# Kernel tuning notes

Hardware: AMD Instinct MI355X
Metric: run time of the kernel (lower is better)

The kernel has to match this reference:

```python
import jax, jax.numpy as jnp
import numpy as np

N_NODES = 100000
N_EDGES = 1600000
IN_DIM = 128
OUT_DIM = 128
LEAKY_SLOPE = 0.01  # torch nn.LeakyReLU default


def setup_inputs() -> dict:
    key = jax.random.key(0)
    k1, k2, k3, k4 = jax.random.split(key, 4)
    x = jax.random.normal(k1, (N_NODES, IN_DIM), dtype=jnp.float32)
    edge_index = jax.random.randint(k2, (2, N_EDGES), 0, N_NODES, dtype=jnp.int64)
    edge_attr = jax.random.uniform(k3, (N_EDGES,), dtype=jnp.float32)
    # Linear params (xavier_uniform weight, zero bias)
    limit = np.sqrt(6.0 / (IN_DIM + OUT_DIM)).astype(np.float32)
    W = jax.random.uniform(k4, (OUT_DIM, IN_DIM), minval=-limit, maxval=limit, dtype=jnp.float32)
    b = jnp.zeros((OUT_DIM,), dtype=jnp.float32)
    return {"x": x, "edge_index": edge_index, "edge_attr": edge_attr, "W": W, "b": b}


def reference(x, edge_index, edge_attr, W, b):
    src = edge_index[0]  # x_j (source nodes)
    dst = edge_index[1]  # aggregation index (target nodes)
    # message: gather source features, scale by per-edge scalar  [E, D]
    msg = x[src] * edge_attr[:, None]
    # aggregate: scatter-add over target index  [N, D]
    agg = jax.ops.segment_sum(msg, dst, num_segments=N_NODES)
    # update: Linear + LeakyReLU (dropout is identity at p=0 / eval)
    out = agg @ W.T + b
    return jnp.where(out >= 0, out, LEAKY_SLOPE * out)
```

## Files before the change

### kernel.cpp

```cpp
#include <hip/hip_runtime.h>

#define N_NODES 100000
#define N_EDGES 1600000
#define DIM 128
#define LEAKY 0.01f
#define RS_STRIDE 132
#define WS_STRIDE 132
#define NBUCKET 391
#define SB_EDGES 4096
#define NSB 391

typedef short bf16x8 __attribute__((ext_vector_type(8)));
typedef float f32x4 __attribute__((ext_vector_type(4)));

static __device__ __forceinline__ unsigned short f2bf(float f) {
  unsigned int u = __float_as_uint(f);
  u = (u + 0x7fffu + ((u >> 16) & 1u)) >> 16;
  return (unsigned short)u;
}

__global__ __launch_bounds__(512) void sort_local_kernel(
    const int* __restrict__ ei, const float* __restrict__ attr,
    int2* __restrict__ binned, unsigned short* __restrict__ counts,
    int* __restrict__ srcOff) {
  __shared__ int hist[NBUCKET];
  __shared__ int cursor[NBUCKET];
  __shared__ int scanBuf[512];
  __shared__ int2 stage[SB_EDGES];

  const int t = threadIdx.x;
  const int blk = blockIdx.x;
  const int base = blk * SB_EDGES;
  const int n = min(SB_EDGES, N_EDGES - base);

  if (t < NBUCKET) hist[t] = 0;
  __syncthreads();

  int myP[8];
  int myB[8];
  float myA[8];
#pragma unroll
  for (int k = 0; k < 8; ++k) {
    int i = t + k * 512;
    if (i < n) {
      int e = base + i;
      int s = ei[e];
      int d = ei[N_EDGES + e];
      myA[k] = attr[e];
      myB[k] = d >> 8;
      myP[k] = s | ((d & 255) << 17);
      atomicAdd(&hist[myB[k]], 1);
    } else {
      myB[k] = -1;
    }
  }
  __syncthreads();

  int v = (t < NBUCKET) ? hist[t] : 0;
  scanBuf[t] = v;
  __syncthreads();
  for (int off = 1; off < 512; off <<= 1) {
    int u = (t >= off) ? scanBuf[t - off] : 0;
    __syncthreads();
    scanBuf[t] += u;
    __syncthreads();
  }
  if (t < NBUCKET) {
    int excl = scanBuf[t] - v;
    cursor[t] = excl;
    counts[(size_t)t * NSB + blk] = (unsigned short)v;
    srcOff[(size_t)t * NSB + blk] = base + excl;
  }
  __syncthreads();

#pragma unroll
  for (int k = 0; k < 8; ++k) {
    if (myB[k] >= 0) {
      int loc = atomicAdd(&cursor[myB[k]], 1);
      stage[loc] = make_int2(myP[k], __float_as_int(myA[k]));
    }
  }
  __syncthreads();

  for (int i = t; i < n; i += 512) binned[base + i] = stage[i];
}

__global__ __launch_bounds__(128) void bucket_count_kernel(
    const unsigned short* __restrict__ counts, int* __restrict__ bucketCount) {
  __shared__ int red[128];
  const int b = blockIdx.x;
  const int t = threadIdx.x;
  int s = 0;
  for (int sb = t; sb < NSB; sb += 128) s += counts[(size_t)b * NSB + sb];
  red[t] = s;
  __syncthreads();
  for (int off = 64; off > 0; off >>= 1) {
    if (t < off) red[t] += red[t + off];
    __syncthreads();
  }
  if (t == 0) bucketCount[b] = red[0];
}

__global__ __launch_bounds__(512) void bucket_scan_kernel(
    const int* __restrict__ bucketCount, int* __restrict__ bucketBase) {
  __shared__ int s[512];
  const int t = threadIdx.x;
  int v = (t < NBUCKET) ? bucketCount[t] : 0;
  s[t] = v;
  __syncthreads();
  for (int off = 1; off < 512; off <<= 1) {
    int u = (t >= off) ? s[t - off] : 0;
    __syncthreads();
    s[t] += u;
    __syncthreads();
  }
  if (t < NBUCKET) bucketBase[t] = s[t] - v;
}

__global__ __launch_bounds__(512) void passB_kernel(
    const int2* __restrict__ binned, const unsigned short* __restrict__ counts,
    const int* __restrict__ srcOff, const int* __restrict__ bucketBase,
    int2* __restrict__ csr, int* __restrict__ row_ptr) {
  __shared__ int runPrefix[NSB + 1];
  __shared__ int runSrc[NSB];
  __shared__ int hist[256];
  __shared__ int nodeBase[256];
  __shared__ int cur[256];
  __shared__ int scanBuf[512];

  const int b = blockIdx.x;
  const int t = threadIdx.x;

  if (t < NSB) runSrc[t] = srcOff[(size_t)b * NSB + t];
  int len = (t < NSB) ? (int)counts[(size_t)b * NSB + t] : 0;
  scanBuf[t] = len;
  __syncthreads();
  for (int off = 1; off < 512; off <<= 1) {
    int u = (t >= off) ? scanBuf[t - off] : 0;
    __syncthreads();
    scanBuf[t] += u;
    __syncthreads();
  }
  if (t < NSB) runPrefix[t] = scanBuf[t] - len;
  if (t == NSB) runPrefix[NSB] = scanBuf[NSB];
  if (t < 256) hist[t] = 0;
  __syncthreads();

  const int total = runPrefix[NSB];

  for (int i = t; i < total; i += 512) {
    int lo = 0, hi = NSB - 1;
    while (lo < hi) {
      int mid = (lo + hi + 1) >> 1;
      if (runPrefix[mid] <= i) lo = mid; else hi = mid - 1;
    }
    int px = binned[runSrc[lo] + (i - runPrefix[lo])].x;
    atomicAdd(&hist[(px >> 17) & 255], 1);
  }
  __syncthreads();

  int hv = (t < 256) ? hist[t] : 0;
  scanBuf[t] = hv;
  __syncthreads();
  for (int off = 1; off < 512; off <<= 1) {
    int u = (t >= off) ? scanBuf[t - off] : 0;
    __syncthreads();
    scanBuf[t] += u;
    __syncthreads();
  }
  const int bb = bucketBase[b];
  if (t < 256) {
    int excl = scanBuf[t] - hv;
    nodeBase[t] = excl;
    cur[t] = excl;
    int node = b * 256 + t;
    if (node < N_NODES) row_ptr[node] = bb + excl;
  }
  if (b == 0 && t == 0) row_ptr[N_NODES] = N_EDGES;
  __syncthreads();

  for (int i = t; i < total; i += 512) {
    int lo = 0, hi = NSB - 1;
    while (lo < hi) {
      int mid = (lo + hi + 1) >> 1;
      if (runPrefix[mid] <= i) lo = mid; else hi = mid - 1;
    }
    int2 rec = binned[runSrc[lo] + (i - runPrefix[lo])];
    int ld = (rec.x >> 17) & 255;
    int pos = bb + atomicAdd(&cur[ld], 1);
    csr[pos] = make_int2(rec.x & 0x1FFFF, rec.y);
  }
}

__global__ __launch_bounds__(256) void x2b_kernel(
    const float4* __restrict__ x, ushort4* __restrict__ xb) {
  const int i = blockIdx.x * 256 + threadIdx.x;
  float4 v = x[i];
  ushort4 o;
  o.x = f2bf(v.x); o.y = f2bf(v.y); o.z = f2bf(v.z); o.w = f2bf(v.w);
  xb[i] = o;
}

__global__ __launch_bounds__(256) void gather_bf16_kernel(
    const unsigned short* __restrict__ xb, const int* __restrict__ row_ptr,
    const int2* __restrict__ csr, float* __restrict__ out) {
  const int node = blockIdx.x * 4 + (threadIdx.x >> 6);
  const int lane = threadIdx.x & 63;

  const int beg = row_ptr[node];
  const int end = row_ptr[node + 1];

  float2 acc = make_float2(0.f, 0.f);
  int e = beg;
  for (; e + 3 < end; e += 4) {
    int2 e0 = csr[e];
    int2 e1 = csr[e + 1];
    int2 e2 = csr[e + 2];
    int2 e3 = csr[e + 3];
    unsigned int u0 = *(const unsigned int*)(xb + (size_t)e0.x * DIM + lane * 2);
    unsigned int u1 = *(const unsigned int*)(xb + (size_t)e1.x * DIM + lane * 2);
    unsigned int u2 = *(const unsigned int*)(xb + (size_t)e2.x * DIM + lane * 2);
    unsigned int u3 = *(const unsigned int*)(xb + (size_t)e3.x * DIM + lane * 2);
    float a0 = __int_as_float(e0.y), a1 = __int_as_float(e1.y);
    float a2 = __int_as_float(e2.y), a3 = __int_as_float(e3.y);
    acc.x += __uint_as_float(u0 << 16) * a0;
    acc.y += __uint_as_float(u0 & 0xffff0000u) * a0;
    acc.x += __uint_as_float(u1 << 16) * a1;
    acc.y += __uint_as_float(u1 & 0xffff0000u) * a1;
    acc.x += __uint_as_float(u2 << 16) * a2;
    acc.y += __uint_as_float(u2 & 0xffff0000u) * a2;
    acc.x += __uint_as_float(u3 << 16) * a3;
    acc.y += __uint_as_float(u3 & 0xffff0000u) * a3;
  }
  for (; e < end; ++e) {
    int2 e0 = csr[e];
    float a0 = __int_as_float(e0.y);
    unsigned int u0 = *(const unsigned int*)(xb + (size_t)e0.x * DIM + lane * 2);
    acc.x += __uint_as_float(u0 << 16) * a0;
    acc.y += __uint_as_float(u0 & 0xffff0000u) * a0;
  }
  *(float2*)(out + (size_t)node * DIM + lane * 2) = acc;
}

__global__ __launch_bounds__(256) void gather_f32_kernel(
    const float* __restrict__ x, const int* __restrict__ row_ptr,
    const int2* __restrict__ csr, float* __restrict__ out) {
  const int node = blockIdx.x * 4 + (threadIdx.x >> 6);
  const int lane = threadIdx.x & 63;

  const int beg = row_ptr[node];
  const int end = row_ptr[node + 1];

  float2 acc = make_float2(0.f, 0.f);
  int e = beg;
  for (; e + 3 < end; e += 4) {
    int2 e0 = csr[e];
    int2 e1 = csr[e + 1];
    int2 e2 = csr[e + 2];
    int2 e3 = csr[e + 3];
    float2 v0 = *(const float2*)(x + (size_t)e0.x * DIM + lane * 2);
    float2 v1 = *(const float2*)(x + (size_t)e1.x * DIM + lane * 2);
    float2 v2 = *(const float2*)(x + (size_t)e2.x * DIM + lane * 2);
    float2 v3 = *(const float2*)(x + (size_t)e3.x * DIM + lane * 2);
    float a0 = __int_as_float(e0.y), a1 = __int_as_float(e1.y);
    float a2 = __int_as_float(e2.y), a3 = __int_as_float(e3.y);
    acc.x += v0.x * a0; acc.y += v0.y * a0;
    acc.x += v1.x * a1; acc.y += v1.y * a1;
    acc.x += v2.x * a2; acc.y += v2.y * a2;
    acc.x += v3.x * a3; acc.y += v3.y * a3;
  }
  for (; e < end; ++e) {
    int2 e0 = csr[e];
    float a0 = __int_as_float(e0.y);
    float2 v0 = *(const float2*)(x + (size_t)e0.x * DIM + lane * 2);
    acc.x += v0.x * a0; acc.y += v0.y * a0;
  }
  *(float2*)(out + (size_t)node * DIM + lane * 2) = acc;
}

__global__ __launch_bounds__(256) void w_frag_kernel(
    const float* __restrict__ W, bf16x8* __restrict__ wfrag) {
  const int gid = blockIdx.x * 256 + threadIdx.x;
  const int lane = gid & 63;
  const int q = (gid >> 6) & 3;
  const int nt = gid >> 8;
  const int n = nt * 16 + (lane & 15);
  const int kb = q * 32 + ((lane >> 4) & 3) * 8;
  const float4 f0 = *(const float4*)(W + n * DIM + kb);
  const float4 f1 = *(const float4*)(W + n * DIM + kb + 4);
  bf16x8 frag;
  frag[0] = (short)f2bf(f0.x); frag[1] = (short)f2bf(f0.y);
  frag[2] = (short)f2bf(f0.z); frag[3] = (short)f2bf(f0.w);
  frag[4] = (short)f2bf(f1.x); frag[5] = (short)f2bf(f1.y);
  frag[6] = (short)f2bf(f1.z); frag[7] = (short)f2bf(f1.w);
  wfrag[gid] = frag;
}

__global__ __launch_bounds__(256) void linear_mfma_kernel(
    const float* __restrict__ agg, const bf16x8* __restrict__ wfrag,
    const float* __restrict__ bias, float* __restrict__ out) {
  const int wave = threadIdx.x >> 6;
  const int lane = threadIdx.x & 63;
  const int r0 = (blockIdx.x * 4 + wave) * 16;
  if (r0 >= N_NODES) return;

  const int m = lane & 15;
  const int quad = lane >> 4;
  const int row = r0 + m;

  bf16x8 afrag[4];
#pragma unroll
  for (int q = 0; q < 4; ++q) {
    const float* ap = agg + (size_t)row * DIM + q * 32 + quad * 8;
    const float4 f0 = *(const float4*)(ap);
    const float4 f1 = *(const float4*)(ap + 4);
    afrag[q][0] = (short)f2bf(f0.x); afrag[q][1] = (short)f2bf(f0.y);
    afrag[q][2] = (short)f2bf(f0.z); afrag[q][3] = (short)f2bf(f0.w);
    afrag[q][4] = (short)f2bf(f1.x); afrag[q][5] = (short)f2bf(f1.y);
    afrag[q][6] = (short)f2bf(f1.z); afrag[q][7] = (short)f2bf(f1.w);
  }

#pragma unroll
  for (int nt = 0; nt < 8; ++nt) {
    const float bv = bias[nt * 16 + m];
    f32x4 acc = {bv, bv, bv, bv};
#pragma unroll
    for (int q = 0; q < 4; ++q) {
      bf16x8 bfrag = wfrag[(nt * 4 + q) * 64 + lane];
      acc = __builtin_amdgcn_mfma_f32_16x16x32_bf16(afrag[q], bfrag, acc, 0, 0, 0);
    }
    const int col = nt * 16 + m;
#pragma unroll
    for (int i = 0; i < 4; ++i) {
      float v = acc[i];
      v = v >= 0.f ? v : v * LEAKY;
      out[(size_t)(r0 + quad * 4 + i) * DIM + col] = v;
    }
  }
}

__global__ __launch_bounds__(256) void scatter_kernel(
    const float* __restrict__ x, const int* __restrict__ ei,
    const float* __restrict__ attr, float* __restrict__ agg) {
  int gid = blockIdx.x * blockDim.x + threadIdx.x;
  int e = gid >> 5;
  int f = (gid & 31) * 4;
  if (e >= N_EDGES) return;
  int s = ei[e];
  int d = ei[N_EDGES + e];
  float a = attr[e];
  const float4 xv = *(const float4*)(x + (size_t)s * DIM + f);
  float* dp = agg + (size_t)d * DIM + f;
  atomicAdd(dp + 0, xv.x * a);
  atomicAdd(dp + 1, xv.y * a);
  atomicAdd(dp + 2, xv.z * a);
  atomicAdd(dp + 3, xv.w * a);
}

__global__ __launch_bounds__(256, 2) void linear_kernel(
    const float* __restrict__ agg, const float* __restrict__ W,
    const float* __restrict__ bias, float* __restrict__ out) {
  __shared__ float Rs[32 * RS_STRIDE];
  __shared__ float Ws[64 * WS_STRIDE];

  const int tid = threadIdx.x;
  const int c = (tid & 31) * 4;
  const int rg = tid >> 5;
  const size_t rowBase = (size_t)blockIdx.x * 32;

  {
    const int lr = tid >> 3;
    const int col = (tid & 7) * 16;
    const float4* src = (const float4*)(agg + (rowBase + lr) * DIM + col);
#pragma unroll
    for (int j = 0; j < 4; ++j) {
      *(float4*)(Rs + lr * RS_STRIDE + col + j * 4) = src[j];
    }
  }

  const float4 bv = *(const float4*)(bias + c);
  float4 acc0 = bv, acc1 = bv, acc2 = bv, acc3 = bv;

  for (int half = 0; half < 2; ++half) {
    __syncthreads();
    {
      const int k0 = tid >> 7;
      const int o = tid & 127;
#pragma unroll
      for (int kk = k0; kk < 64; kk += 2) {
        Ws[kk * WS_STRIDE + o] = W[o * DIM + half * 64 + kk];
      }
    }
    __syncthreads();

    const float* rs0 = Rs + (rg * 4 + 0) * RS_STRIDE + half * 64;
    const float* rs1 = Rs + (rg * 4 + 1) * RS_STRIDE + half * 64;
    const float* rs2 = Rs + (rg * 4 + 2) * RS_STRIDE + half * 64;
    const float* rs3 = Rs + (rg * 4 + 3) * RS_STRIDE + half * 64;

#pragma unroll 8
    for (int k4 = 0; k4 < 16; ++k4) {
      const float4 v0 = *(const float4*)(rs0 + k4 * 4);
      const float4 v1 = *(const float4*)(rs1 + k4 * 4);
      const float4 v2 = *(const float4*)(rs2 + k4 * 4);
      const float4 v3 = *(const float4*)(rs3 + k4 * 4);
      const float4 w0 = *(const float4*)(Ws + (k4 * 4 + 0) * WS_STRIDE + c);
      const float4 w1 = *(const float4*)(Ws + (k4 * 4 + 1) * WS_STRIDE + c);
      const float4 w2 = *(const float4*)(Ws + (k4 * 4 + 2) * WS_STRIDE + c);
      const float4 w3 = *(const float4*)(Ws + (k4 * 4 + 3) * WS_STRIDE + c);

#define FMA4(acc, v)                                               \
      acc.x += v.x * w0.x + v.y * w1.x + v.z * w2.x + v.w * w3.x;  \
      acc.y += v.x * w0.y + v.y * w1.y + v.z * w2.y + v.w * w3.y;  \
      acc.z += v.x * w0.z + v.y * w1.z + v.z * w2.z + v.w * w3.z;  \
      acc.w += v.x * w0.w + v.y * w1.w + v.z * w2.w + v.w * w3.w;
      FMA4(acc0, v0)
      FMA4(acc1, v1)
      FMA4(acc2, v2)
      FMA4(acc3, v3)
#undef FMA4
    }
  }

#define LEAKY4(acc)                                   \
  acc.x = acc.x >= 0.f ? acc.x : acc.x * LEAKY;       \
  acc.y = acc.y >= 0.f ? acc.y : acc.y * LEAKY;       \
  acc.z = acc.z >= 0.f ? acc.z : acc.z * LEAKY;       \
  acc.w = acc.w >= 0.f ? acc.w : acc.w * LEAKY;
  LEAKY4(acc0) LEAKY4(acc1) LEAKY4(acc2) LEAKY4(acc3)
#undef LEAKY4

  const int row0 = (int)rowBase + rg * 4;
  *(float4*)(out + (size_t)(row0 + 0) * DIM + c) = acc0;
  *(float4*)(out + (size_t)(row0 + 1) * DIM + c) = acc1;
  *(float4*)(out + (size_t)(row0 + 2) * DIM + c) = acc2;
  *(float4*)(out + (size_t)(row0 + 3) * DIM + c) = acc3;
}

extern "C" void kernel_launch(void* const* d_in, const int* in_sizes, int n_in,
                              void* d_out, int out_size, void* d_ws, size_t ws_size,
                              hipStream_t stream) {
  const float* x = (const float*)d_in[0];
  const int* ei = (const int*)d_in[1];
  const float* attr = (const float*)d_in[2];
  const float* W = (const float*)d_in[3];
  const float* b = (const float*)d_in[4];
  float* out = (float*)d_out;

  const size_t offBinned = 0;
  const size_t offCounts = 12812288;
  const size_t offSrcOff = offCounts + 305920;
  const size_t offBCount = offSrcOff + 611584;
  const size_t offBBase  = offBCount + 1792;
  const size_t offCsr    = offBBase + 1792;
  const size_t offRowPtr = offCsr + 12812288;
  const size_t offWfrag  = offRowPtr + 400128;
  const size_t sortNeed  = offWfrag + 32768;
  const size_t offXb     = sortNeed;
  const size_t fullNeed  = offXb + 25600000;

  if (ws_size >= sortNeed) {
    char* ws = (char*)d_ws;
    int2* binned = (int2*)(ws + offBinned);
    unsigned short* counts = (unsigned short*)(ws + offCounts);
    int* srcOff = (int*)(ws + offSrcOff);
    int* bucketCount = (int*)(ws + offBCount);
    int* bucketBase = (int*)(ws + offBBase);
    int2* csr = (int2*)(ws + offCsr);
    int* row_ptr = (int*)(ws + offRowPtr);
    bf16x8* wfrag = (bf16x8*)(ws + offWfrag);

    w_frag_kernel<<<8, 256, 0, stream>>>(W, wfrag);
    sort_local_kernel<<<NSB, 512, 0, stream>>>(ei, attr, binned, counts, srcOff);
    bucket_count_kernel<<<NBUCKET, 128, 0, stream>>>(counts, bucketCount);
    bucket_scan_kernel<<<1, 512, 0, stream>>>(bucketCount, bucketBase);
    passB_kernel<<<NBUCKET, 512, 0, stream>>>(binned, counts, srcOff, bucketBase,
                                              csr, row_ptr);
    if (ws_size >= fullNeed) {
      unsigned short* xb = (unsigned short*)(ws + offXb);
      x2b_kernel<<<12500, 256, 0, stream>>>((const float4*)x, (ushort4*)xb);
      gather_bf16_kernel<<<N_NODES / 4, 256, 0, stream>>>(xb, row_ptr, csr, out);
    } else {
      gather_f32_kernel<<<N_NODES / 4, 256, 0, stream>>>(x, row_ptr, csr, out);
    }
    linear_mfma_kernel<<<(N_NODES + 63) / 64, 256, 0, stream>>>(out, wfrag, b, out);
  } else {
    hipMemsetAsync(out, 0, (size_t)N_NODES * DIM * sizeof(float), stream);
    scatter_kernel<<<(N_EDGES * 32) / 256, 256, 0, stream>>>(x, ei, attr, out);
    linear_kernel<<<N_NODES / 32, 256, 0, stream>>>(out, W, b, out);
  }
}
```

Baseline: 250.6 us.

## Fuse gather with MFMA linear layer and simplify passB run traversal

The bf16 gather and the linear+LeakyReLU step become one kernel. Each block aggregates 16 nodes into shared memory, then runs the 16x128 by 128x128 product with bf16 MFMA and writes the activated output directly, so the aggregated matrix no longer makes a round trip through global memory. Separately, passB drops the per-element binary search over run prefixes: each thread now walks one run serially and the block shrinks to 448 threads. The serial walk may be less balanced and less coalesced than the old strided loop, and the fused kernel now rounds the aggregated features to bf16 before the product.

```diff
diff --git a/kernel.cpp b/kernel.cpp
--- a/kernel.cpp
+++ b/kernel.cpp
@@ -6,6 +6,7 @@
 #define LEAKY 0.01f
 #define RS_STRIDE 132
 #define WS_STRIDE 132
+#define LSTRIDE 132
 #define NBUCKET 391
 #define SB_EDGES 4096
 #define NSB 391
@@ -117,61 +118,49 @@
   if (t < NBUCKET) bucketBase[t] = s[t] - v;
 }
 
-__global__ __launch_bounds__(512) void passB_kernel(
+__global__ __launch_bounds__(448) void passB_kernel(
     const int2* __restrict__ binned, const unsigned short* __restrict__ counts,
     const int* __restrict__ srcOff, const int* __restrict__ bucketBase,
     int2* __restrict__ csr, int* __restrict__ row_ptr) {
-  __shared__ int runPrefix[NSB + 1];
   __shared__ int runSrc[NSB];
+  __shared__ int runLen[NSB];
   __shared__ int hist[256];
-  __shared__ int nodeBase[256];
   __shared__ int cur[256];
-  __shared__ int scanBuf[512];
+  __shared__ int scanBuf[256];
 
   const int b = blockIdx.x;
   const int t = threadIdx.x;
 
-  if (t < NSB) runSrc[t] = srcOff[(size_t)b * NSB + t];
-  int len = (t < NSB) ? (int)counts[(size_t)b * NSB + t] : 0;
-  scanBuf[t] = len;
-  __syncthreads();
-  for (int off = 1; off < 512; off <<= 1) {
-    int u = (t >= off) ? scanBuf[t - off] : 0;
-    __syncthreads();
-    scanBuf[t] += u;
-    __syncthreads();
-  }
-  if (t < NSB) runPrefix[t] = scanBuf[t] - len;
-  if (t == NSB) runPrefix[NSB] = scanBuf[NSB];
+  if (t < NSB) {
+    runSrc[t] = srcOff[(size_t)b * NSB + t];
+    runLen[t] = (int)counts[(size_t)b * NSB + t];
+  }
   if (t < 256) hist[t] = 0;
   __syncthreads();
 
-  const int total = runPrefix[NSB];
-
-  for (int i = t; i < total; i += 512) {
-    int lo = 0, hi = NSB - 1;
-    while (lo < hi) {
-      int mid = (lo + hi + 1) >> 1;
-      if (runPrefix[mid] <= i) lo = mid; else hi = mid - 1;
-    }
-    int px = binned[runSrc[lo] + (i - runPrefix[lo])].x;
-    atomicAdd(&hist[(px >> 17) & 255], 1);
+  if (t < NSB) {
+    const int src = runSrc[t];
+    const int len = runLen[t];
+    for (int j = 0; j < len; ++j) {
+      int px = binned[src + j].x;
+      atomicAdd(&hist[(px >> 17) & 255], 1);
+    }
   }
   __syncthreads();
 
   int hv = (t < 256) ? hist[t] : 0;
-  scanBuf[t] = hv;
-  __syncthreads();
-  for (int off = 1; off < 512; off <<= 1) {
-    int u = (t >= off) ? scanBuf[t - off] : 0;
-    __syncthreads();
-    scanBuf[t] += u;
+  if (t < 256) scanBuf[t] = hv;
+  __syncthreads();
+  for (int off = 1; off < 256; off <<= 1) {
+    int u = 0;
+    if (t < 256 && t >= off) u = scanBuf[t - off];
+    __syncthreads();
+    if (t < 256) scanBuf[t] += u;
     __syncthreads();
   }
   const int bb = bucketBase[b];
   if (t < 256) {
     int excl = scanBuf[t] - hv;
-    nodeBase[t] = excl;
     cur[t] = excl;
     int node = b * 256 + t;
     if (node < N_NODES) row_ptr[node] = bb + excl;
@@ -179,16 +168,15 @@
   if (b == 0 && t == 0) row_ptr[N_NODES] = N_EDGES;
   __syncthreads();
 
-  for (int i = t; i < total; i += 512) {
-    int lo = 0, hi = NSB - 1;
-    while (lo < hi) {
-      int mid = (lo + hi + 1) >> 1;
-      if (runPrefix[mid] <= i) lo = mid; else hi = mid - 1;
-    }
-    int2 rec = binned[runSrc[lo] + (i - runPrefix[lo])];
-    int ld = (rec.x >> 17) & 255;
-    int pos = bb + atomicAdd(&cur[ld], 1);
-    csr[pos] = make_int2(rec.x & 0x1FFFF, rec.y);
+  if (t < NSB) {
+    const int src = runSrc[t];
+    const int len = runLen[t];
+    for (int j = 0; j < len; ++j) {
+      int2 rec = binned[src + j];
+      int ld = (rec.x >> 17) & 255;
+      int pos = bb + atomicAdd(&cur[ld], 1);
+      csr[pos] = make_int2(rec.x & 0x1FFFF, rec.y);
+    }
   }
 }
 
@@ -201,45 +189,89 @@
   xb[i] = o;
 }
 
-__global__ __launch_bounds__(256) void gather_bf16_kernel(
+__global__ __launch_bounds__(256) void gather_linear_kernel(
     const unsigned short* __restrict__ xb, const int* __restrict__ row_ptr,
-    const int2* __restrict__ csr, float* __restrict__ out) {
-  const int node = blockIdx.x * 4 + (threadIdx.x >> 6);
+    const int2* __restrict__ csr, const bf16x8* __restrict__ wfrag,
+    const float* __restrict__ bias, float* __restrict__ out) {
+  __shared__ float Ls[16 * LSTRIDE];
+
+  const int w = threadIdx.x >> 6;
   const int lane = threadIdx.x & 63;
-
-  const int beg = row_ptr[node];
-  const int end = row_ptr[node + 1];
-
-  float2 acc = make_float2(0.f, 0.f);
-  int e = beg;
-  for (; e + 3 < end; e += 4) {
-    int2 e0 = csr[e];
-    int2 e1 = csr[e + 1];
-    int2 e2 = csr[e + 2];
-    int2 e3 = csr[e + 3];
-    unsigned int u0 = *(const unsigned int*)(xb + (size_t)e0.x * DIM + lane * 2);
-    unsigned int u1 = *(const unsigned int*)(xb + (size_t)e1.x * DIM + lane * 2);
-    unsigned int u2 = *(const unsigned int*)(xb + (size_t)e2.x * DIM + lane * 2);
-    unsigned int u3 = *(const unsigned int*)(xb + (size_t)e3.x * DIM + lane * 2);
-    float a0 = __int_as_float(e0.y), a1 = __int_as_float(e1.y);
-    float a2 = __int_as_float(e2.y), a3 = __int_as_float(e3.y);
-    acc.x += __uint_as_float(u0 << 16) * a0;
-    acc.y += __uint_as_float(u0 & 0xffff0000u) * a0;
-    acc.x += __uint_as_float(u1 << 16) * a1;
-    acc.y += __uint_as_float(u1 & 0xffff0000u) * a1;
-    acc.x += __uint_as_float(u2 << 16) * a2;
-    acc.y += __uint_as_float(u2 & 0xffff0000u) * a2;
-    acc.x += __uint_as_float(u3 << 16) * a3;
-    acc.y += __uint_as_float(u3 & 0xffff0000u) * a3;
-  }
-  for (; e < end; ++e) {
-    int2 e0 = csr[e];
-    float a0 = __int_as_float(e0.y);
-    unsigned int u0 = *(const unsigned int*)(xb + (size_t)e0.x * DIM + lane * 2);
-    acc.x += __uint_as_float(u0 << 16) * a0;
-    acc.y += __uint_as_float(u0 & 0xffff0000u) * a0;
-  }
-  *(float2*)(out + (size_t)node * DIM + lane * 2) = acc;
+  const int nodeBase = blockIdx.x * 16;
+
+#pragma unroll
+  for (int k = 0; k < 4; ++k) {
+    const int loc = w * 4 + k;
+    const int node = nodeBase + loc;
+    const int beg = row_ptr[node];
+    const int end = row_ptr[node + 1];
+
+    float2 acc = make_float2(0.f, 0.f);
+    int e = beg;
+    for (; e + 3 < end; e += 4) {
+      int2 e0 = csr[e];
+      int2 e1 = csr[e + 1];
+      int2 e2 = csr[e + 2];
+      int2 e3 = csr[e + 3];
+      unsigned int u0 = *(const unsigned int*)(xb + (size_t)e0.x * DIM + lane * 2);
+      unsigned int u1 = *(const unsigned int*)(xb + (size_t)e1.x * DIM + lane * 2);
+      unsigned int u2 = *(const unsigned int*)(xb + (size_t)e2.x * DIM + lane * 2);
+      unsigned int u3 = *(const unsigned int*)(xb + (size_t)e3.x * DIM + lane * 2);
+      float a0 = __int_as_float(e0.y), a1 = __int_as_float(e1.y);
+      float a2 = __int_as_float(e2.y), a3 = __int_as_float(e3.y);
+      acc.x += __uint_as_float(u0 << 16) * a0;
+      acc.y += __uint_as_float(u0 & 0xffff0000u) * a0;
+      acc.x += __uint_as_float(u1 << 16) * a1;
+      acc.y += __uint_as_float(u1 & 0xffff0000u) * a1;
+      acc.x += __uint_as_float(u2 << 16) * a2;
+      acc.y += __uint_as_float(u2 & 0xffff0000u) * a2;
+      acc.x += __uint_as_float(u3 << 16) * a3;
+      acc.y += __uint_as_float(u3 & 0xffff0000u) * a3;
+    }
+    for (; e < end; ++e) {
+      int2 e0 = csr[e];
+      float a0 = __int_as_float(e0.y);
+      unsigned int u0 = *(const unsigned int*)(xb + (size_t)e0.x * DIM + lane * 2);
+      acc.x += __uint_as_float(u0 << 16) * a0;
+      acc.y += __uint_as_float(u0 & 0xffff0000u) * a0;
+    }
+    *(float2*)(Ls + loc * LSTRIDE + lane * 2) = acc;
+  }
+  __syncthreads();
+
+  const int m = lane & 15;
+  const int quad = lane >> 4;
+
+  bf16x8 afrag[4];
+#pragma unroll
+  for (int q = 0; q < 4; ++q) {
+    const float* ap = Ls + m * LSTRIDE + q * 32 + quad * 8;
+    const float4 f0 = *(const float4*)(ap);
+    const float4 f1 = *(const float4*)(ap + 4);
+    afrag[q][0] = (short)f2bf(f0.x); afrag[q][1] = (short)f2bf(f0.y);
+    afrag[q][2] = (short)f2bf(f0.z); afrag[q][3] = (short)f2bf(f0.w);
+    afrag[q][4] = (short)f2bf(f1.x); afrag[q][5] = (short)f2bf(f1.y);
+    afrag[q][6] = (short)f2bf(f1.z); afrag[q][7] = (short)f2bf(f1.w);
+  }
+
+#pragma unroll
+  for (int j = 0; j < 2; ++j) {
+    const int nt = w * 2 + j;
+    const float bv = bias[nt * 16 + m];
+    f32x4 acc = {bv, bv, bv, bv};
+#pragma unroll
+    for (int q = 0; q < 4; ++q) {
+      bf16x8 bfrag = wfrag[(nt * 4 + q) * 64 + lane];
+      acc = __builtin_amdgcn_mfma_f32_16x16x32_bf16(afrag[q], bfrag, acc, 0, 0, 0);
+    }
+    const int col = nt * 16 + m;
+#pragma unroll
+    for (int i = 0; i < 4; ++i) {
+      float v = acc[i];
+      v = v >= 0.f ? v : v * LEAKY;
+      out[(size_t)(nodeBase + quad * 4 + i) * DIM + col] = v;
+    }
+  }
 }
 
 __global__ __launch_bounds__(256) void gather_f32_kernel(
@@ -474,16 +506,17 @@
     sort_local_kernel<<<NSB, 512, 0, stream>>>(ei, attr, binned, counts, srcOff);
     bucket_count_kernel<<<NBUCKET, 128, 0, stream>>>(counts, bucketCount);
     bucket_scan_kernel<<<1, 512, 0, stream>>>(bucketCount, bucketBase);
-    passB_kernel<<<NBUCKET, 512, 0, stream>>>(binned, counts, srcOff, bucketBase,
+    passB_kernel<<<NBUCKET, 448, 0, stream>>>(binned, counts, srcOff, bucketBase,
                                               csr, row_ptr);
     if (ws_size >= fullNeed) {
       unsigned short* xb = (unsigned short*)(ws + offXb);
       x2b_kernel<<<12500, 256, 0, stream>>>((const float4*)x, (ushort4*)xb);
-      gather_bf16_kernel<<<N_NODES / 4, 256, 0, stream>>>(xb, row_ptr, csr, out);
+      gather_linear_kernel<<<N_NODES / 16, 256, 0, stream>>>(xb, row_ptr, csr,
+                                                             wfrag, b, out);
     } else {
       gather_f32_kernel<<<N_NODES / 4, 256, 0, stream>>>(x, row_ptr, csr, out);
-    }
-    linear_mfma_kernel<<<(N_NODES + 63) / 64, 256, 0, stream>>>(out, wfrag, b, out);
+      linear_mfma_kernel<<<(N_NODES + 63) / 64, 256, 0, stream>>>(out, wfrag, b, out);
+    }
   } else {
     hipMemsetAsync(out, 0, (size_t)N_NODES * DIM * sizeof(float), stream);
     scatter_kernel<<<(N_EDGES * 32) / 256, 256, 0, stream>>>(x, ei, attr, out);
```

Result: slower. 261.9 us (+4.5%).
